# Performance work log

Hardware: AMD Instinct MI355X
Metric: run time of the kernel (lower is better)

Reference implementation:

```python
import jax, jax.numpy as jnp
import numpy as np

D = 768  # hidden dim hard-coded in the module


def setup_inputs() -> dict:
    key = jax.random.key(0)
    k1, k2, k3, k4, k5 = jax.random.split(key, 5)
    N, M = 512, 512
    return {
        "text_output": jax.random.normal(k1, (N, D), dtype=jnp.float32),
        "visual_output": jax.random.normal(k2, (M, D), dtype=jnp.float32),
        "W1": jax.random.normal(k3, (D, D), dtype=jnp.float32),
        "W2": jax.random.normal(k4, (D, D), dtype=jnp.float32),
        "W3": jax.random.normal(k5, (D, D), dtype=jnp.float32),
    }


def reference(text_output, visual_output, W1, W2, W3):
    # C[n,m] = tanh( (text @ W1) . visual[m] )
    C = jnp.tanh((text_output @ W1) @ visual_output.T)            # (N, M)
    W2_text = text_output @ W2                                    # (N, D)
    W3_visual = visual_output @ W3.T                              # (M, D)
    # M[n,m,:] = tanh(W2_text[n] + W3_visual[m] * C[n,m])
    Mt = jnp.tanh(W2_text[:, None, :] + W3_visual[None, :, :] * C[..., None])  # (N, M, D)
    # score[n,m] = text[n] . M[n,m]  (replaces the per-row Python loop)
    score = jnp.einsum("nd,nmd->nm", text_output, Mt)             # (N, M)
    return score
```

## Files before the change

### kernel.cpp

```cpp
#include <hip/hip_runtime.h>

#define DD   768
#define NN   512
#define MM   512

#define PRE_K 2.88539008177792681472f

typedef _Float16 h8 __attribute__((ext_vector_type(8)));
typedef __attribute__((ext_vector_type(4))) float f32x4;

__device__ __forceinline__ float fexp(float x) { return __builtin_amdgcn_exp2f(x); }
__device__ __forceinline__ float frcp(float x) { return __builtin_amdgcn_rcpf(x); }
__device__ __forceinline__ float fast_tanh(float x) {
  return 1.0f - 2.0f * frcp(fexp(PRE_K * x) + 1.0f);
}

__device__ __forceinline__ void splitf(float x, ushort& h, ushort& l) {
  const _Float16 hh = (_Float16)x;
  const _Float16 ll = (_Float16)(x - (float)hh);
  h = __builtin_bit_cast(unsigned short, hh);
  l = __builtin_bit_cast(unsigned short, ll);
}

__global__ __launch_bounds__(256) void prep_kernel(
    const float* __restrict__ text, const float* __restrict__ visual,
    const float* __restrict__ W1, const float* __restrict__ W2,
    const float* __restrict__ W3,
    ushort* __restrict__ th, ushort* __restrict__ tl,
    ushort* __restrict__ vh, ushort* __restrict__ vl,
    ushort* __restrict__ w3h, ushort* __restrict__ w3l,
    ushort* __restrict__ w1th, ushort* __restrict__ w1tl,
    ushort* __restrict__ w2th, ushort* __restrict__ w2tl,
    float* __restrict__ out)
{
  __shared__ float Lt[32][33];
  const int b = blockIdx.x;
  const int t = threadIdx.x;

  if (b < 1344) {
    const float* src; ushort *dh, *dl; size_t off;
    if (b < 384)      { src = text;   dh = th;  dl = tl;  off = (size_t)b * 1024; }
    else if (b < 768) { src = visual; dh = vh;  dl = vl;  off = (size_t)(b - 384) * 1024; }
    else              { src = W3;     dh = w3h; dl = w3l; off = (size_t)(b - 768) * 1024; }
    const size_t i = off + (size_t)t * 4;
    const float4 v = *(const float4*)&src[i];
    ushort4 h, l;
    splitf(v.x, h.x, l.x); splitf(v.y, h.y, l.y);
    splitf(v.z, h.z, l.z); splitf(v.w, h.w, l.w);
    *(ushort4*)&dh[i] = h;
    *(ushort4*)&dl[i] = l;
  } else if (b < 2496) {
    const int tt = b - 1344;
    const bool second = tt >= 576;
    const int tile = second ? tt - 576 : tt;
    const float* W = second ? W2 : W1;
    ushort* oh = second ? w2th : w1th;
    ushort* ol = second ? w2tl : w1tl;
    const int k0 = (tile / 24) * 32, j0 = (tile % 24) * 32;
    {
      const int k = t >> 3, j4 = (t & 7) * 4;
      const float4 v = *(const float4*)&W[(size_t)(k0 + k) * DD + j0 + j4];
      Lt[j4 + 0][k] = v.x; Lt[j4 + 1][k] = v.y;
      Lt[j4 + 2][k] = v.z; Lt[j4 + 3][k] = v.w;
    }
    __syncthreads();
    {
      const int j = t >> 3, k4 = (t & 7) * 4;
      ushort4 h, l;
      splitf(Lt[j][k4 + 0], h.x, l.x); splitf(Lt[j][k4 + 1], h.y, l.y);
      splitf(Lt[j][k4 + 2], h.z, l.z); splitf(Lt[j][k4 + 3], h.w, l.w);
      *(ushort4*)&oh[(size_t)(j0 + j) * DD + k0 + k4] = h;
      *(ushort4*)&ol[(size_t)(j0 + j) * DD + k0 + k4] = l;
    }
  } else {
    float* red = (float*)Lt;
    const int u = b - 2496;
    const int n0 = u * 2;
    const int half = t >> 7;
    const int lt = t & 127;

    const float* tr = text + (size_t)(n0 + half) * DD;
    float s = 0.f;
    #pragma unroll
    for (int i = 0; i < DD / 128; ++i) s += tr[lt + i * 128];
    red[t] = s;
    __syncthreads();
    #pragma unroll
    for (int st = 64; st > 0; st >>= 1) {
      if (lt < st) red[t] += red[t + st];
      __syncthreads();
    }
    const float Tn = red[half << 7];
    float4 o; o.x = Tn; o.y = Tn; o.z = Tn; o.w = Tn;
    *(float4*)&out[(size_t)(n0 + half) * MM + lt * 4] = o;
  }
}

#define BK   32
#define LROW 40
#define APL  (32 * LROW)
#define BPL  (64 * LROW)

template <bool ALO>
__device__ __forceinline__ void gemm_core32(
    ushort* __restrict__ As, ushort* __restrict__ Bs,
    const ushort* __restrict__ Ahg, const ushort* __restrict__ Alg,
    const ushort* __restrict__ Bhg, const ushort* __restrict__ Blg,
    int i0, int j0, int nsteps, f32x4* acc)
{
  const int tid = threadIdx.x;
  const int row = tid >> 2;
  const int ks8 = (tid & 3) * 8;
  const bool doA = (row < 32);
  const size_t ga = (size_t)(i0 + row) * DD + ks8;
  const size_t gb = (size_t)(j0 + row) * DD + ks8;
  const int lw = row * LROW + ks8;

  const int lane = tid & 63, wave = tid >> 6;
  const int r15 = lane & 15, quad = lane >> 4;
  const int wr = wave >> 1, wc = wave & 1;
  const int fa = (wr * 16 + r15) * LROW + quad * 8;
  const int fb = (wc * 32 + r15) * LROW + quad * 8;

  h8 pah, pal, pbh, pbl;
  if (doA) {
    pah = *(const h8*)(Ahg + ga);
    if (ALO) pal = *(const h8*)(Alg + ga);
  }
  pbh = *(const h8*)(Bhg + gb);
  pbl = *(const h8*)(Blg + gb);

  int p = 0;
  if (doA) {
    *(h8*)&As[lw] = pah;
    if (ALO) *(h8*)&As[APL + lw] = pal;
  }
  *(h8*)&Bs[lw] = pbh;
  *(h8*)&Bs[BPL + lw] = pbl;
  __syncthreads();

  for (int s = 0; s < nsteps; ++s) {
    const bool more = (s + 1 < nsteps);
    if (more) {
      if (doA) {
        pah = *(const h8*)(Ahg + ga + (s + 1) * BK);
        if (ALO) pal = *(const h8*)(Alg + ga + (s + 1) * BK);
      }
      pbh = *(const h8*)(Bhg + gb + (s + 1) * BK);
      pbl = *(const h8*)(Blg + gb + (s + 1) * BK);
    }
    ushort* Ac = As + p * 2 * APL;
    ushort* Bc = Bs + p * 2 * BPL;
    const h8 a_h = *(const h8*)&Ac[fa];
    h8 a_l; if (ALO) a_l = *(const h8*)&Ac[APL + fa];
    h8 b_h[2], b_l[2];
    #pragma unroll
    for (int c = 0; c < 2; ++c) {
      b_h[c] = *(const h8*)&Bc[fb + c * 16 * LROW];
      b_l[c] = *(const h8*)&Bc[BPL + fb + c * 16 * LROW];
    }
    #pragma unroll
    for (int c = 0; c < 2; ++c)
      acc[c] = __builtin_amdgcn_mfma_f32_16x16x32_f16(a_h, b_h[c], acc[c], 0, 0, 0);
    #pragma unroll
    for (int c = 0; c < 2; ++c)
      acc[c] = __builtin_amdgcn_mfma_f32_16x16x32_f16(a_h, b_l[c], acc[c], 0, 0, 0);
    if (ALO) {
      #pragma unroll
      for (int c = 0; c < 2; ++c)
        acc[c] = __builtin_amdgcn_mfma_f32_16x16x32_f16(a_l, b_h[c], acc[c], 0, 0, 0);
    }
    if (more) {
      const int q = p ^ 1;
      ushort* An = As + q * 2 * APL;
      ushort* Bn = Bs + q * 2 * BPL;
      if (doA) {
        *(h8*)&An[lw] = pah;
        if (ALO) *(h8*)&An[APL + lw] = pal;
      }
      *(h8*)&Bn[lw] = pbh;
      *(h8*)&Bn[BPL + lw] = pbl;
    }
    __syncthreads();
    p ^= 1;
  }
}

__global__ __launch_bounds__(256) void mfma1_kernel(
    const ushort* __restrict__ th, const ushort* __restrict__ tl,
    const ushort* __restrict__ vh, const ushort* __restrict__ vl,
    const ushort* __restrict__ w1th, const ushort* __restrict__ w1tl,
    const ushort* __restrict__ w2th, const ushort* __restrict__ w2tl,
    const ushort* __restrict__ w3h, const ushort* __restrict__ w3l,
    ushort* __restrict__ Ah, ushort* __restrict__ Al,
    float* __restrict__ kw2t, float* __restrict__ kw3v)
{
  __shared__ ushort As[2 * 2 * APL];
  __shared__ ushort Bs[2 * 2 * BPL];

  const int z  = blockIdx.z;
  const int j0 = blockIdx.x * 64;
  const int i0 = blockIdx.y * 32;

  f32x4 acc[2];
  acc[0] = (f32x4){0.f, 0.f, 0.f, 0.f};
  acc[1] = (f32x4){0.f, 0.f, 0.f, 0.f};

  if (z == 0)
    gemm_core32<true >(As, Bs, th, tl, w1th, w1tl, i0, j0, DD / BK, acc);
  else if (z == 1)
    gemm_core32<false>(As, Bs, th, tl, w2th, w2tl, i0, j0, DD / BK, acc);
  else
    gemm_core32<false>(As, Bs, vh, vl, w3h,  w3l,  i0, j0, DD / BK, acc);

  const int lane = threadIdx.x & 63, wave = threadIdx.x >> 6;
  const int r15 = lane & 15, quad = lane >> 4;
  const int wr = wave >> 1, wc = wave & 1;
  if (z == 0) {
    #pragma unroll
    for (int c = 0; c < 2; ++c)
      #pragma unroll
      for (int r = 0; r < 4; ++r) {
        const size_t o = (size_t)(i0 + wr * 16 + quad * 4 + r) * DD
                       + j0 + wc * 32 + c * 16 + r15;
        splitf(acc[c][r], Ah[o], Al[o]);
      }
  } else {
    float* Out = (z == 1) ? kw2t : kw3v;
    #pragma unroll
    for (int c = 0; c < 2; ++c)
      #pragma unroll
      for (int r = 0; r < 4; ++r)
        Out[(size_t)(i0 + wr * 16 + quad * 4 + r) * DD + j0 + wc * 32 + c * 16 + r15] =
            acc[c][r] * PRE_K;
  }
}

#define DCH    64
#define DRANGE 256
#define MLDW   68

__global__ __launch_bounds__(256) void main_kernel(
    const float* __restrict__ text, const float* __restrict__ kw2t,
    const float* __restrict__ kw3v,
    const ushort* __restrict__ Ah, const ushort* __restrict__ Al,
    const ushort* __restrict__ vh, const ushort* __restrict__ vl,
    float* __restrict__ out)
{
  __shared__ float sbuf[2][32 * MLDW];

  const int tid = threadIdx.x;
  const int nl = tid >> 4;
  const int ml = tid & 15;
  const int n0 = blockIdx.y * 16;
  const int m0 = blockIdx.x * 32;
  const int z  = blockIdx.z;
  const int lane = tid & 63, wave = tid >> 6;
  const int r15 = lane & 15, quad = lane >> 4;

  const size_t aoff  = (size_t)(n0 + r15) * DD + wave * (DD / 4) + quad * 8;
  const size_t b0off = (size_t)(m0 + r15) * DD + wave * (DD / 4) + quad * 8;
  const size_t b1off = (size_t)(m0 + 16 + r15) * DD + wave * (DD / 4) + quad * 8;
  const ushort* Ap  = Ah + aoff;
  const ushort* Alp = Al + aoff;
  const ushort* B0h = vh + b0off;
  const ushort* B0l = vl + b0off;
  const ushort* B1h = vh + b1off;
  const ushort* B1l = vl + b1off;

  f32x4 q0 = {0.f, 0.f, 0.f, 0.f}, q1 = {0.f, 0.f, 0.f, 0.f};
  h8 cah  = *(const h8*)Ap;
  h8 cal  = *(const h8*)Alp;
  h8 cb0h = *(const h8*)B0h;
  h8 cb0l = *(const h8*)B0l;
  h8 cb1h = *(const h8*)B1h;
  h8 cb1l = *(const h8*)B1l;
  #pragma unroll
  for (int s = 0; s < (DD / 4) / BK; ++s) {
    h8 nah, nal, nb0h, nb0l, nb1h, nb1l;
    const bool more = (s + 1 < (DD / 4) / BK);
    if (more) {
      nah  = *(const h8*)(Ap  + (s + 1) * BK);
      nal  = *(const h8*)(Alp + (s + 1) * BK);
      nb0h = *(const h8*)(B0h + (s + 1) * BK);
      nb0l = *(const h8*)(B0l + (s + 1) * BK);
      nb1h = *(const h8*)(B1h + (s + 1) * BK);
      nb1l = *(const h8*)(B1l + (s + 1) * BK);
    }
    q0 = __builtin_amdgcn_mfma_f32_16x16x32_f16(cah, cb0h, q0, 0, 0, 0);
    q1 = __builtin_amdgcn_mfma_f32_16x16x32_f16(cah, cb1h, q1, 0, 0, 0);
    q0 = __builtin_amdgcn_mfma_f32_16x16x32_f16(cah, cb0l, q0, 0, 0, 0);
    q1 = __builtin_amdgcn_mfma_f32_16x16x32_f16(cah, cb1l, q1, 0, 0, 0);
    q0 = __builtin_amdgcn_mfma_f32_16x16x32_f16(cal, cb0h, q0, 0, 0, 0);
    q1 = __builtin_amdgcn_mfma_f32_16x16x32_f16(cal, cb1h, q1, 0, 0, 0);
    if (more) { cah = nah; cal = nal; cb0h = nb0h; cb0l = nb0l; cb1h = nb1h; cb1l = nb1l; }
  }

  float (*Qs)[16][33] = (float (*)[16][33])(&sbuf[0][0]);
  #pragma unroll
  for (int r = 0; r < 4; ++r) {
    Qs[wave][quad * 4 + r][r15]      = q0[r];
    Qs[wave][quad * 4 + r][16 + r15] = q1[r];
  }
  __syncthreads();
  float sA = Qs[0][nl][ml];
  sA += Qs[1][nl][ml]; sA += Qs[2][nl][ml]; sA += Qs[3][nl][ml];
  float sB = Qs[0][nl][ml + 16];
  sB += Qs[1][nl][ml + 16]; sB += Qs[2][nl][ml + 16]; sB += Qs[3][nl][ml + 16];
  const float cA = fast_tanh(sA);
  const float cB = fast_tanh(sB);
  __syncthreads();

  const int n  = n0 + nl;
  const int mA = m0 + ml, mB = mA + 16;
  const int dbase = z * DRANGE;

  float4 aA = {0.f, 0.f, 0.f, 0.f};
  float4 aB = {0.f, 0.f, 0.f, 0.f};

  const float* gt = &text[(size_t)n * DD + dbase];
  const float* g2 = &kw2t[(size_t)n * DD + dbase];

  const int srow = tid >> 4;
  const int sc4  = (tid & 15) << 2;
  const float* g3a = &kw3v[(size_t)(m0 + srow) * DD + dbase + sc4];
  const float* g3b = &kw3v[(size_t)(m0 + 16 + srow) * DD + dbase + sc4];
  const int w3a = srow * MLDW + sc4;
  const int w3b = (16 + srow) * MLDW + sc4;

  float4 r3a = *(const float4*)g3a;
  float4 r3b = *(const float4*)g3b;
  int p = 0;
  *(float4*)&sbuf[0][w3a] = r3a;
  *(float4*)&sbuf[0][w3b] = r3b;
  __syncthreads();

  #pragma unroll
  for (int c = 0; c < DRANGE / DCH; ++c) {
    const bool more = (c + 1 < DRANGE / DCH);
    if (more) {
      r3a = *(const float4*)(g3a + (c + 1) * DCH);
      r3b = *(const float4*)(g3b + (c + 1) * DCH);
    }
    const float* bp = sbuf[p];
    const float* gtc = gt + c * DCH;
    const float* g2c = g2 + c * DCH;
    #pragma unroll 4
    for (int j = 0; j < DCH; j += 4) {
      const float4 tv  = *(const float4*)&gtc[j];
      const float4 w2v = *(const float4*)&g2c[j];
      const float4 w3A = *(const float4*)&bp[ml * MLDW + j];
      const float4 w3B = *(const float4*)&bp[(16 + ml) * MLDW + j];
      aA.x = fmaf(tv.x, frcp(fexp(fmaf(w3A.x, cA, w2v.x)) + 1.0f), aA.x);
      aA.y = fmaf(tv.y, frcp(fexp(fmaf(w3A.y, cA, w2v.y)) + 1.0f), aA.y);
      aA.z = fmaf(tv.z, frcp(fexp(fmaf(w3A.z, cA, w2v.z)) + 1.0f), aA.z);
      aA.w = fmaf(tv.w, frcp(fexp(fmaf(w3A.w, cA, w2v.w)) + 1.0f), aA.w);
      aB.x = fmaf(tv.x, frcp(fexp(fmaf(w3B.x, cB, w2v.x)) + 1.0f), aB.x);
      aB.y = fmaf(tv.y, frcp(fexp(fmaf(w3B.y, cB, w2v.y)) + 1.0f), aB.y);
      aB.z = fmaf(tv.z, frcp(fexp(fmaf(w3B.z, cB, w2v.z)) + 1.0f), aB.z);
      aB.w = fmaf(tv.w, frcp(fexp(fmaf(w3B.w, cB, w2v.w)) + 1.0f), aB.w);
    }
    if (more) {
      const int q = p ^ 1;
      *(float4*)&sbuf[q][w3a] = r3a;
      *(float4*)&sbuf[q][w3b] = r3b;
    }
    __syncthreads();
    p ^= 1;
  }

  float* op = out + (size_t)n * MM;
  unsafeAtomicAdd(&op[mA], -2.0f * ((aA.x + aA.y) + (aA.z + aA.w)));
  unsafeAtomicAdd(&op[mB], -2.0f * ((aB.x + aB.y) + (aB.z + aB.w)));
}

extern "C" void kernel_launch(void* const* d_in, const int* in_sizes, int n_in,
                              void* d_out, int out_size, void* d_ws, size_t ws_size,
                              hipStream_t stream) {
  const float* text   = (const float*)d_in[0];
  const float* visual = (const float*)d_in[1];
  const float* W1     = (const float*)d_in[2];
  const float* W2     = (const float*)d_in[3];
  const float* W3     = (const float*)d_in[4];
  float* out = (float*)d_out;

  char* base = (char*)d_ws;
  ushort* th   = (ushort*)(base);
  ushort* tl   = (ushort*)(base + 786432);
  ushort* vh   = (ushort*)(base + 1572864);
  ushort* vl   = (ushort*)(base + 2359296);
  ushort* w1th = (ushort*)(base + 3145728);
  ushort* w1tl = (ushort*)(base + 4325376);
  ushort* w2th = (ushort*)(base + 5505024);
  ushort* w2tl = (ushort*)(base + 6684672);
  ushort* w3h  = (ushort*)(base + 7864320);
  ushort* w3l  = (ushort*)(base + 9043968);
  ushort* Ah   = (ushort*)(base + 10223616);
  ushort* Al   = (ushort*)(base + 11010048);
  float*  kw2t = (float*) (base + 11796480);
  float*  kw3v = (float*) (base + 13369344);

  hipLaunchKernelGGL(prep_kernel, dim3(2752), dim3(256), 0, stream,
                     text, visual, W1, W2, W3,
                     th, tl, vh, vl, w3h, w3l, w1th, w1tl, w2th, w2tl, out);
  hipLaunchKernelGGL(mfma1_kernel, dim3(DD / 64, NN / 32, 3), dim3(256), 0, stream,
                     th, tl, vh, vl, w1th, w1tl, w2th, w2tl, w3h, w3l,
                     Ah, Al, kw2t, kw3v);
  hipLaunchKernelGGL(main_kernel, dim3(MM / 32, NN / 16, 3), dim3(256), 0, stream,
                     text, kw2t, kw3v, Ah, Al, vh, vl, out);
}
```

Before: 142.3 us.

## Merge three kernels into one cooperative persistent kernel with grid syncs

New measurement: 480.0 us. 237% more time.

```diff
diff --git a/kernel.cpp b/kernel.cpp
--- a/kernel.cpp
+++ b/kernel.cpp
@@ -1,4 +1,7 @@
 #include <hip/hip_runtime.h>
+#include <hip/hip_cooperative_groups.h>
+
+namespace cg = cooperative_groups;
 
 #define DD   768
 #define NN   512
@@ -22,80 +25,6 @@
   l = __builtin_bit_cast(unsigned short, ll);
 }
 
-__global__ __launch_bounds__(256) void prep_kernel(
-    const float* __restrict__ text, const float* __restrict__ visual,
-    const float* __restrict__ W1, const float* __restrict__ W2,
-    const float* __restrict__ W3,
-    ushort* __restrict__ th, ushort* __restrict__ tl,
-    ushort* __restrict__ vh, ushort* __restrict__ vl,
-    ushort* __restrict__ w3h, ushort* __restrict__ w3l,
-    ushort* __restrict__ w1th, ushort* __restrict__ w1tl,
-    ushort* __restrict__ w2th, ushort* __restrict__ w2tl,
-    float* __restrict__ out)
-{
-  __shared__ float Lt[32][33];
-  const int b = blockIdx.x;
-  const int t = threadIdx.x;
-
-  if (b < 1344) {
-    const float* src; ushort *dh, *dl; size_t off;
-    if (b < 384)      { src = text;   dh = th;  dl = tl;  off = (size_t)b * 1024; }
-    else if (b < 768) { src = visual; dh = vh;  dl = vl;  off = (size_t)(b - 384) * 1024; }
-    else              { src = W3;     dh = w3h; dl = w3l; off = (size_t)(b - 768) * 1024; }
-    const size_t i = off + (size_t)t * 4;
-    const float4 v = *(const float4*)&src[i];
-    ushort4 h, l;
-    splitf(v.x, h.x, l.x); splitf(v.y, h.y, l.y);
-    splitf(v.z, h.z, l.z); splitf(v.w, h.w, l.w);
-    *(ushort4*)&dh[i] = h;
-    *(ushort4*)&dl[i] = l;
-  } else if (b < 2496) {
-    const int tt = b - 1344;
-    const bool second = tt >= 576;
-    const int tile = second ? tt - 576 : tt;
-    const float* W = second ? W2 : W1;
-    ushort* oh = second ? w2th : w1th;
-    ushort* ol = second ? w2tl : w1tl;
-    const int k0 = (tile / 24) * 32, j0 = (tile % 24) * 32;
-    {
-      const int k = t >> 3, j4 = (t & 7) * 4;
-      const float4 v = *(const float4*)&W[(size_t)(k0 + k) * DD + j0 + j4];
-      Lt[j4 + 0][k] = v.x; Lt[j4 + 1][k] = v.y;
-      Lt[j4 + 2][k] = v.z; Lt[j4 + 3][k] = v.w;
-    }
-    __syncthreads();
-    {
-      const int j = t >> 3, k4 = (t & 7) * 4;
-      ushort4 h, l;
-      splitf(Lt[j][k4 + 0], h.x, l.x); splitf(Lt[j][k4 + 1], h.y, l.y);
-      splitf(Lt[j][k4 + 2], h.z, l.z); splitf(Lt[j][k4 + 3], h.w, l.w);
-      *(ushort4*)&oh[(size_t)(j0 + j) * DD + k0 + k4] = h;
-      *(ushort4*)&ol[(size_t)(j0 + j) * DD + k0 + k4] = l;
-    }
-  } else {
-    float* red = (float*)Lt;
-    const int u = b - 2496;
-    const int n0 = u * 2;
-    const int half = t >> 7;
-    const int lt = t & 127;
-
-    const float* tr = text + (size_t)(n0 + half) * DD;
-    float s = 0.f;
-    #pragma unroll
-    for (int i = 0; i < DD / 128; ++i) s += tr[lt + i * 128];
-    red[t] = s;
-    __syncthreads();
-    #pragma unroll
-    for (int st = 64; st > 0; st >>= 1) {
-      if (lt < st) red[t] += red[t + st];
-      __syncthreads();
-    }
-    const float Tn = red[half << 7];
-    float4 o; o.x = Tn; o.y = Tn; o.z = Tn; o.w = Tn;
-    *(float4*)&out[(size_t)(n0 + half) * MM + lt * 4] = o;
-  }
-}
-
 #define BK   32
 #define LROW 40
 #define APL  (32 * LROW)
@@ -103,17 +32,17 @@
 
 template <bool ALO>
 __device__ __forceinline__ void gemm_core32(
-    ushort* __restrict__ As, ushort* __restrict__ Bs,
-    const ushort* __restrict__ Ahg, const ushort* __restrict__ Alg,
-    const ushort* __restrict__ Bhg, const ushort* __restrict__ Blg,
-    int i0, int j0, int nsteps, f32x4* acc)
+    ushort* As, ushort* Bs,
+    const ushort* Ahg, const ushort* Alg,
+    const ushort* Bhg, const ushort* Blg,
+    int i0, int j0, int k0, int nsteps, f32x4* acc)
 {
   const int tid = threadIdx.x;
   const int row = tid >> 2;
   const int ks8 = (tid & 3) * 8;
   const bool doA = (row < 32);
-  const size_t ga = (size_t)(i0 + row) * DD + ks8;
-  const size_t gb = (size_t)(j0 + row) * DD + ks8;
+  const size_t ga = (size_t)(i0 + row) * DD + k0 + ks8;
+  const size_t gb = (size_t)(j0 + row) * DD + k0 + ks8;
   const int lw = row * LROW + ks8;
 
   const int lane = tid & 63, wave = tid >> 6;
@@ -186,192 +115,249 @@
   }
 }
 
-__global__ __launch_bounds__(256) void mfma1_kernel(
-    const ushort* __restrict__ th, const ushort* __restrict__ tl,
-    const ushort* __restrict__ vh, const ushort* __restrict__ vl,
-    const ushort* __restrict__ w1th, const ushort* __restrict__ w1tl,
-    const ushort* __restrict__ w2th, const ushort* __restrict__ w2tl,
-    const ushort* __restrict__ w3h, const ushort* __restrict__ w3l,
+#define DCH    64
+#define DRANGE 192
+#define MLDW   68
+#define SMEM_BYTES 34816
+
+__global__ __launch_bounds__(256, 4) void mega_kernel(
+    const float* __restrict__ text, const float* __restrict__ visual,
+    const float* __restrict__ W1, const float* __restrict__ W2,
+    const float* __restrict__ W3,
+    ushort* __restrict__ th, ushort* __restrict__ tl,
+    ushort* __restrict__ vh, ushort* __restrict__ vl,
+    ushort* __restrict__ w3h, ushort* __restrict__ w3l,
+    ushort* w1th, ushort* w1tl,
+    ushort* w2th, ushort* w2tl,
     ushort* __restrict__ Ah, ushort* __restrict__ Al,
-    float* __restrict__ kw2t, float* __restrict__ kw3v)
-{
-  __shared__ ushort As[2 * 2 * APL];
-  __shared__ ushort Bs[2 * 2 * BPL];
-
-  const int z  = blockIdx.z;
-  const int j0 = blockIdx.x * 64;
-  const int i0 = blockIdx.y * 32;
-
-  f32x4 acc[2];
-  acc[0] = (f32x4){0.f, 0.f, 0.f, 0.f};
-  acc[1] = (f32x4){0.f, 0.f, 0.f, 0.f};
-
-  if (z == 0)
-    gemm_core32<true >(As, Bs, th, tl, w1th, w1tl, i0, j0, DD / BK, acc);
-  else if (z == 1)
-    gemm_core32<false>(As, Bs, th, tl, w2th, w2tl, i0, j0, DD / BK, acc);
-  else
-    gemm_core32<false>(As, Bs, vh, vl, w3h,  w3l,  i0, j0, DD / BK, acc);
-
-  const int lane = threadIdx.x & 63, wave = threadIdx.x >> 6;
-  const int r15 = lane & 15, quad = lane >> 4;
-  const int wr = wave >> 1, wc = wave & 1;
-  if (z == 0) {
-    #pragma unroll
-    for (int c = 0; c < 2; ++c)
-      #pragma unroll
-      for (int r = 0; r < 4; ++r) {
-        const size_t o = (size_t)(i0 + wr * 16 + quad * 4 + r) * DD
-                       + j0 + wc * 32 + c * 16 + r15;
-        splitf(acc[c][r], Ah[o], Al[o]);
-      }
-  } else {
-    float* Out = (z == 1) ? kw2t : kw3v;
-    #pragma unroll
-    for (int c = 0; c < 2; ++c)
-      #pragma unroll
-      for (int r = 0; r < 4; ++r)
-        Out[(size_t)(i0 + wr * 16 + quad * 4 + r) * DD + j0 + wc * 32 + c * 16 + r15] =
-            acc[c][r] * PRE_K;
-  }
-}
-
-#define DCH    64
-#define DRANGE 256
-#define MLDW   68
-
-__global__ __launch_bounds__(256) void main_kernel(
-    const float* __restrict__ text, const float* __restrict__ kw2t,
-    const float* __restrict__ kw3v,
-    const ushort* __restrict__ Ah, const ushort* __restrict__ Al,
-    const ushort* __restrict__ vh, const ushort* __restrict__ vl,
+    float* __restrict__ kw2t, float* __restrict__ kw3v,
+    float* Q,
     float* __restrict__ out)
 {
-  __shared__ float sbuf[2][32 * MLDW];
-
-  const int tid = threadIdx.x;
-  const int nl = tid >> 4;
-  const int ml = tid & 15;
-  const int n0 = blockIdx.y * 16;
-  const int m0 = blockIdx.x * 32;
-  const int z  = blockIdx.z;
-  const int lane = tid & 63, wave = tid >> 6;
-  const int r15 = lane & 15, quad = lane >> 4;
-
-  const size_t aoff  = (size_t)(n0 + r15) * DD + wave * (DD / 4) + quad * 8;
-  const size_t b0off = (size_t)(m0 + r15) * DD + wave * (DD / 4) + quad * 8;
-  const size_t b1off = (size_t)(m0 + 16 + r15) * DD + wave * (DD / 4) + quad * 8;
-  const ushort* Ap  = Ah + aoff;
-  const ushort* Alp = Al + aoff;
-  const ushort* B0h = vh + b0off;
-  const ushort* B0l = vl + b0off;
-  const ushort* B1h = vh + b1off;
-  const ushort* B1l = vl + b1off;
-
-  f32x4 q0 = {0.f, 0.f, 0.f, 0.f}, q1 = {0.f, 0.f, 0.f, 0.f};
-  h8 cah  = *(const h8*)Ap;
-  h8 cal  = *(const h8*)Alp;
-  h8 cb0h = *(const h8*)B0h;
-  h8 cb0l = *(const h8*)B0l;
-  h8 cb1h = *(const h8*)B1h;
-  h8 cb1l = *(const h8*)B1l;
-  #pragma unroll
-  for (int s = 0; s < (DD / 4) / BK; ++s) {
-    h8 nah, nal, nb0h, nb0l, nb1h, nb1l;
-    const bool more = (s + 1 < (DD / 4) / BK);
-    if (more) {
-      nah  = *(const h8*)(Ap  + (s + 1) * BK);
-      nal  = *(const h8*)(Alp + (s + 1) * BK);
-      nb0h = *(const h8*)(B0h + (s + 1) * BK);
-      nb0l = *(const h8*)(B0l + (s + 1) * BK);
-      nb1h = *(const h8*)(B1h + (s + 1) * BK);
-      nb1l = *(const h8*)(B1l + (s + 1) * BK);
-    }
-    q0 = __builtin_amdgcn_mfma_f32_16x16x32_f16(cah, cb0h, q0, 0, 0, 0);
-    q1 = __builtin_amdgcn_mfma_f32_16x16x32_f16(cah, cb1h, q1, 0, 0, 0);
-    q0 = __builtin_amdgcn_mfma_f32_16x16x32_f16(cah, cb0l, q0, 0, 0, 0);
-    q1 = __builtin_amdgcn_mfma_f32_16x16x32_f16(cah, cb1l, q1, 0, 0, 0);
-    q0 = __builtin_amdgcn_mfma_f32_16x16x32_f16(cal, cb0h, q0, 0, 0, 0);
-    q1 = __builtin_amdgcn_mfma_f32_16x16x32_f16(cal, cb1h, q1, 0, 0, 0);
-    if (more) { cah = nah; cal = nal; cb0h = nb0h; cb0l = nb0l; cb1h = nb1h; cb1l = nb1l; }
-  }
-
-  float (*Qs)[16][33] = (float (*)[16][33])(&sbuf[0][0]);
-  #pragma unroll
-  for (int r = 0; r < 4; ++r) {
-    Qs[wave][quad * 4 + r][r15]      = q0[r];
-    Qs[wave][quad * 4 + r][16 + r15] = q1[r];
-  }
-  __syncthreads();
-  float sA = Qs[0][nl][ml];
-  sA += Qs[1][nl][ml]; sA += Qs[2][nl][ml]; sA += Qs[3][nl][ml];
-  float sB = Qs[0][nl][ml + 16];
-  sB += Qs[1][nl][ml + 16]; sB += Qs[2][nl][ml + 16]; sB += Qs[3][nl][ml + 16];
-  const float cA = fast_tanh(sA);
-  const float cB = fast_tanh(sB);
-  __syncthreads();
-
-  const int n  = n0 + nl;
-  const int mA = m0 + ml, mB = mA + 16;
-  const int dbase = z * DRANGE;
-
-  float4 aA = {0.f, 0.f, 0.f, 0.f};
-  float4 aB = {0.f, 0.f, 0.f, 0.f};
-
-  const float* gt = &text[(size_t)n * DD + dbase];
-  const float* g2 = &kw2t[(size_t)n * DD + dbase];
-
-  const int srow = tid >> 4;
-  const int sc4  = (tid & 15) << 2;
-  const float* g3a = &kw3v[(size_t)(m0 + srow) * DD + dbase + sc4];
-  const float* g3b = &kw3v[(size_t)(m0 + 16 + srow) * DD + dbase + sc4];
-  const int w3a = srow * MLDW + sc4;
-  const int w3b = (16 + srow) * MLDW + sc4;
-
-  float4 r3a = *(const float4*)g3a;
-  float4 r3b = *(const float4*)g3b;
-  int p = 0;
-  *(float4*)&sbuf[0][w3a] = r3a;
-  *(float4*)&sbuf[0][w3b] = r3b;
-  __syncthreads();
-
-  #pragma unroll
-  for (int c = 0; c < DRANGE / DCH; ++c) {
-    const bool more = (c + 1 < DRANGE / DCH);
-    if (more) {
-      r3a = *(const float4*)(g3a + (c + 1) * DCH);
-      r3b = *(const float4*)(g3b + (c + 1) * DCH);
-    }
-    const float* bp = sbuf[p];
-    const float* gtc = gt + c * DCH;
-    const float* g2c = g2 + c * DCH;
-    #pragma unroll 4
-    for (int j = 0; j < DCH; j += 4) {
-      const float4 tv  = *(const float4*)&gtc[j];
-      const float4 w2v = *(const float4*)&g2c[j];
-      const float4 w3A = *(const float4*)&bp[ml * MLDW + j];
-      const float4 w3B = *(const float4*)&bp[(16 + ml) * MLDW + j];
-      aA.x = fmaf(tv.x, frcp(fexp(fmaf(w3A.x, cA, w2v.x)) + 1.0f), aA.x);
-      aA.y = fmaf(tv.y, frcp(fexp(fmaf(w3A.y, cA, w2v.y)) + 1.0f), aA.y);
-      aA.z = fmaf(tv.z, frcp(fexp(fmaf(w3A.z, cA, w2v.z)) + 1.0f), aA.z);
-      aA.w = fmaf(tv.w, frcp(fexp(fmaf(w3A.w, cA, w2v.w)) + 1.0f), aA.w);
-      aB.x = fmaf(tv.x, frcp(fexp(fmaf(w3B.x, cB, w2v.x)) + 1.0f), aB.x);
-      aB.y = fmaf(tv.y, frcp(fexp(fmaf(w3B.y, cB, w2v.y)) + 1.0f), aB.y);
-      aB.z = fmaf(tv.z, frcp(fexp(fmaf(w3B.z, cB, w2v.z)) + 1.0f), aB.z);
-      aB.w = fmaf(tv.w, frcp(fexp(fmaf(w3B.w, cB, w2v.w)) + 1.0f), aB.w);
-    }
-    if (more) {
-      const int q = p ^ 1;
-      *(float4*)&sbuf[q][w3a] = r3a;
-      *(float4*)&sbuf[q][w3b] = r3b;
-    }
-    __syncthreads();
-    p ^= 1;
-  }
-
-  float* op = out + (size_t)n * MM;
-  unsafeAtomicAdd(&op[mA], -2.0f * ((aA.x + aA.y) + (aA.z + aA.w)));
-  unsafeAtomicAdd(&op[mB], -2.0f * ((aB.x + aB.y) + (aB.z + aB.w)));
+  __shared__ __align__(16) char smem[SMEM_BYTES];
+  cg::grid_group grid = cg::this_grid();
+  const int t  = threadIdx.x;
+  const int nb = gridDim.x;
+
+  {
+    float (*Lt)[33] = (float (*)[33])smem;
+    for (int b = blockIdx.x; b < 2752; b += nb) {
+      if (b < 1344) {
+        const float* src; ushort *dh, *dl; size_t off;
+        if (b < 384)      { src = text;   dh = th;  dl = tl;  off = (size_t)b * 1024; }
+        else if (b < 768) { src = visual; dh = vh;  dl = vl;  off = (size_t)(b - 384) * 1024; }
+        else              { src = W3;     dh = w3h; dl = w3l; off = (size_t)(b - 768) * 1024; }
+        const size_t i = off + (size_t)t * 4;
+        const float4 v = *(const float4*)&src[i];
+        ushort4 h, l;
+        splitf(v.x, h.x, l.x); splitf(v.y, h.y, l.y);
+        splitf(v.z, h.z, l.z); splitf(v.w, h.w, l.w);
+        *(ushort4*)&dh[i] = h;
+        *(ushort4*)&dl[i] = l;
+      } else if (b < 2496) {
+        const int tt = b - 1344;
+        const bool second = tt >= 576;
+        const int tile = second ? tt - 576 : tt;
+        const float* W = second ? W2 : W1;
+        ushort* oh = second ? w2th : w1th;
+        ushort* ol = second ? w2tl : w1tl;
+        const int k0 = (tile / 24) * 32, j0 = (tile % 24) * 32;
+        {
+          const int k = t >> 3, j4 = (t & 7) * 4;
+          const float4 v = *(const float4*)&W[(size_t)(k0 + k) * DD + j0 + j4];
+          Lt[j4 + 0][k] = v.x; Lt[j4 + 1][k] = v.y;
+          Lt[j4 + 2][k] = v.z; Lt[j4 + 3][k] = v.w;
+        }
+        __syncthreads();
+        {
+          const int j = t >> 3, k4 = (t & 7) * 4;
+          ushort4 h, l;
+          splitf(Lt[j][k4 + 0], h.x, l.x); splitf(Lt[j][k4 + 1], h.y, l.y);
+          splitf(Lt[j][k4 + 2], h.z, l.z); splitf(Lt[j][k4 + 3], h.w, l.w);
+          *(ushort4*)&oh[(size_t)(j0 + j) * DD + k0 + k4] = h;
+          *(ushort4*)&ol[(size_t)(j0 + j) * DD + k0 + k4] = l;
+        }
+      } else {
+        float* red = (float*)smem;
+        const int u = b - 2496;
+        const int n0 = u * 2;
+        const int half = t >> 7;
+        const int lt = t & 127;
+        const float* tr = text + (size_t)(n0 + half) * DD;
+        float s = 0.f;
+        #pragma unroll
+        for (int i = 0; i < DD / 128; ++i) s += tr[lt + i * 128];
+        red[t] = s;
+        __syncthreads();
+        #pragma unroll
+        for (int st = 64; st > 0; st >>= 1) {
+          if (lt < st) red[t] += red[t + st];
+          __syncthreads();
+        }
+        const float Tn = red[half << 7];
+        float4 o; o.x = Tn; o.y = Tn; o.z = Tn; o.w = Tn;
+        *(float4*)&out[(size_t)(n0 + half) * MM + lt * 4] = o;
+      }
+      __syncthreads();
+    }
+  }
+  __threadfence();
+  grid.sync();
+
+  {
+    ushort* As = (ushort*)smem;
+    ushort* Bs = (ushort*)(smem + 10240);
+    const int lane = t & 63, wave = t >> 6;
+    const int r15 = lane & 15, quad = lane >> 4;
+    const int wr = wave >> 1, wc = wave & 1;
+    for (int u = blockIdx.x; u < 576; u += nb) {
+      const int z = u / 192, rem = u % 192;
+      const int j0 = (rem % 12) * 64, i0 = (rem / 12) * 32;
+      f32x4 acc[2];
+      acc[0] = (f32x4){0.f, 0.f, 0.f, 0.f};
+      acc[1] = (f32x4){0.f, 0.f, 0.f, 0.f};
+      if (z == 0)
+        gemm_core32<true >(As, Bs, th, tl, w1th, w1tl, i0, j0, 0, DD / BK, acc);
+      else if (z == 1)
+        gemm_core32<false>(As, Bs, th, tl, w2th, w2tl, i0, j0, 0, DD / BK, acc);
+      else
+        gemm_core32<false>(As, Bs, vh, vl, w3h,  w3l,  i0, j0, 0, DD / BK, acc);
+      if (z == 0) {
+        #pragma unroll
+        for (int c = 0; c < 2; ++c)
+          #pragma unroll
+          for (int r = 0; r < 4; ++r) {
+            const size_t o = (size_t)(i0 + wr * 16 + quad * 4 + r) * DD
+                           + j0 + wc * 32 + c * 16 + r15;
+            splitf(acc[c][r], Ah[o], Al[o]);
+          }
+      } else {
+        float* Out = (z == 1) ? kw2t : kw3v;
+        #pragma unroll
+        for (int c = 0; c < 2; ++c)
+          #pragma unroll
+          for (int r = 0; r < 4; ++r)
+            Out[(size_t)(i0 + wr * 16 + quad * 4 + r) * DD + j0 + wc * 32 + c * 16 + r15] =
+                acc[c][r] * PRE_K;
+      }
+    }
+  }
+  __threadfence();
+  grid.sync();
+
+  {
+    ushort* As = (ushort*)smem;
+    ushort* Bs = (ushort*)(smem + 10240);
+    const int lane = t & 63, wave = t >> 6;
+    const int r15 = lane & 15, quad = lane >> 4;
+    const int wr = wave >> 1, wc = wave & 1;
+    for (int u = blockIdx.x; u < 512; u += nb) {
+      const int z = u >> 7, rem = u & 127;
+      const int j0 = (rem & 7) * 64, i0 = (rem >> 3) * 32;
+      f32x4 acc[2];
+      acc[0] = (f32x4){0.f, 0.f, 0.f, 0.f};
+      acc[1] = (f32x4){0.f, 0.f, 0.f, 0.f};
+      gemm_core32<true>(As, Bs, Ah, Al, vh, vl, i0, j0, z * (DD / 4), (DD / 4) / BK, acc);
+      float* Qp = Q + (size_t)z * NN * MM;
+      #pragma unroll
+      for (int c = 0; c < 2; ++c)
+        #pragma unroll
+        for (int r = 0; r < 4; ++r)
+          Qp[(size_t)(i0 + wr * 16 + quad * 4 + r) * MM + j0 + wc * 32 + c * 16 + r15] =
+              acc[c][r];
+    }
+  }
+  __threadfence();
+  grid.sync();
+
+  {
+    float* sb = (float*)smem;
+    const int nl = t >> 4;
+    const int ml = t & 15;
+    for (int u = blockIdx.x; u < 2048; u += nb) {
+      const int z  = u >> 9;
+      const int rem = u & 511;
+      const int m0 = (rem & 15) * 32;
+      const int n0 = (rem >> 4) * 16;
+      const int n  = n0 + nl;
+      const int mA = m0 + ml, mB = mA + 16;
+      const int dbase = z * DRANGE;
+
+      float cA = 0.f, cB = 0.f;
+      #pragma unroll
+      for (int zz = 0; zz < 4; ++zz) {
+        const float* q = Q + (size_t)zz * NN * MM + (size_t)n * MM;
+        cA += q[mA]; cB += q[mB];
+      }
+      cA = fast_tanh(cA); cB = fast_tanh(cB);
+
+      float4 aA = {0.f, 0.f, 0.f, 0.f};
+      float4 aB = {0.f, 0.f, 0.f, 0.f};
+
+      const int srow = t >> 4;
+      const int sc4  = (t & 15) << 2;
+      const float* gt  = &text[(size_t)(n0 + srow) * DD + dbase + sc4];
+      const float* g2  = &kw2t[(size_t)(n0 + srow) * DD + dbase + sc4];
+      const float* g3a = &kw3v[(size_t)(m0 + srow) * DD + dbase + sc4];
+      const float* g3b = &kw3v[(size_t)(m0 + 16 + srow) * DD + dbase + sc4];
+      const int wt  = srow * MLDW + sc4;
+      const int w2  = (16 + srow) * MLDW + sc4;
+      const int w3a = (32 + srow) * MLDW + sc4;
+      const int w3b = (48 + srow) * MLDW + sc4;
+
+      float4 rt  = *(const float4*)gt;
+      float4 r2  = *(const float4*)g2;
+      float4 r3a = *(const float4*)g3a;
+      float4 r3b = *(const float4*)g3b;
+      int p = 0;
+      *(float4*)&sb[wt]  = rt;
+      *(float4*)&sb[w2]  = r2;
+      *(float4*)&sb[w3a] = r3a;
+      *(float4*)&sb[w3b] = r3b;
+      __syncthreads();
+
+      #pragma unroll
+      for (int c = 0; c < DRANGE / DCH; ++c) {
+        const bool more = (c + 1 < DRANGE / DCH);
+        if (more) {
+          rt  = *(const float4*)(gt  + (c + 1) * DCH);
+          r2  = *(const float4*)(g2  + (c + 1) * DCH);
+          r3a = *(const float4*)(g3a + (c + 1) * DCH);
+          r3b = *(const float4*)(g3b + (c + 1) * DCH);
+        }
+        const float* bp = sb + p * (64 * MLDW);
+        #pragma unroll 4
+        for (int j = 0; j < DCH; j += 4) {
+          const float4 tv  = *(const float4*)&bp[nl * MLDW + j];
+          const float4 w2v = *(const float4*)&bp[(16 + nl) * MLDW + j];
+          const float4 w3A = *(const float4*)&bp[(32 + ml) * MLDW + j];
+          const float4 w3B = *(const float4*)&bp[(48 + ml) * MLDW + j];
+          aA.x = fmaf(tv.x, frcp(fexp(fmaf(w3A.x, cA, w2v.x)) + 1.0f), aA.x);
+          aA.y = fmaf(tv.y, frcp(fexp(fmaf(w3A.y, cA, w2v.y)) + 1.0f), aA.y);
+          aA.z = fmaf(tv.z, frcp(fexp(fmaf(w3A.z, cA, w2v.z)) + 1.0f), aA.z);
+          aA.w = fmaf(tv.w, frcp(fexp(fmaf(w3A.w, cA, w2v.w)) + 1.0f), aA.w);
+          aB.x = fmaf(tv.x, frcp(fexp(fmaf(w3B.x, cB, w2v.x)) + 1.0f), aB.x);
+          aB.y = fmaf(tv.y, frcp(fexp(fmaf(w3B.y, cB, w2v.y)) + 1.0f), aB.y);
+          aB.z = fmaf(tv.z, frcp(fexp(fmaf(w3B.z, cB, w2v.z)) + 1.0f), aB.z);
+          aB.w = fmaf(tv.w, frcp(fexp(fmaf(w3B.w, cB, w2v.w)) + 1.0f), aB.w);
+        }
+        if (more) {
+          const int q = p ^ 1;
+          float* nbuf = sb + q * (64 * MLDW);
+          *(float4*)&nbuf[wt]  = rt;
+          *(float4*)&nbuf[w2]  = r2;
+          *(float4*)&nbuf[w3a] = r3a;
+          *(float4*)&nbuf[w3b] = r3b;
+        }
+        __syncthreads();
+        p ^= 1;
+      }
+
+      float* op = out + (size_t)n * MM;
+      unsafeAtomicAdd(&op[mA], -2.0f * ((aA.x + aA.y) + (aA.z + aA.w)));
+      unsafeAtomicAdd(&op[mB], -2.0f * ((aB.x + aB.y) + (aB.z + aB.w)));
+    }
+  }
 }
 
 extern "C" void kernel_launch(void* const* d_in, const int* in_sizes, int n_in,
@@ -399,13 +385,22 @@
   ushort* Al   = (ushort*)(base + 11010048);
   float*  kw2t = (float*) (base + 11796480);
   float*  kw3v = (float*) (base + 13369344);
-
-  hipLaunchKernelGGL(prep_kernel, dim3(2752), dim3(256), 0, stream,
-                     text, visual, W1, W2, W3,
-                     th, tl, vh, vl, w3h, w3l, w1th, w1tl, w2th, w2tl, out);
-  hipLaunchKernelGGL(mfma1_kernel, dim3(DD / 64, NN / 32, 3), dim3(256), 0, stream,
-                     th, tl, vh, vl, w1th, w1tl, w2th, w2tl, w3h, w3l,
-                     Ah, Al, kw2t, kw3v);
-  hipLaunchKernelGGL(main_kernel, dim3(MM / 32, NN / 16, 3), dim3(256), 0, stream,
-                     text, kw2t, kw3v, Ah, Al, vh, vl, out);
+  float*  Q    = (ws_size >= (size_t)19136512) ? (float*)(base + 14942208)
+                                               : (float*)(base + 3145728);
+
+  int maxb = 0;
+  hipOccupancyMaxActiveBlocksPerMultiprocessor(&maxb, mega_kernel, 256, 0);
+  if (maxb < 1) maxb = 1;
+  int grid = maxb * 256;
+  if (grid > 1024) grid = 1024;
+
+  void* args[] = {
+    (void*)&text, (void*)&visual, (void*)&W1, (void*)&W2, (void*)&W3,
+    (void*)&th, (void*)&tl, (void*)&vh, (void*)&vl,
+    (void*)&w3h, (void*)&w3l, (void*)&w1th, (void*)&w1tl,
+    (void*)&w2th, (void*)&w2tl, (void*)&Ah, (void*)&Al,
+    (void*)&kw2t, (void*)&kw3v, (void*)&Q, (void*)&out
+  };
+  hipLaunchCooperativeKernel((const void*)mega_kernel, dim3(grid), dim3(256),
+                             args, 0, stream);
 }
```

## Split C-score GEMM into separate split-K kernel and stage text/W2 in LDS

Applied to the files above, without the earlier changes.

Measured after the change: 145.0 us. Within noise of the previous version (+1.9%).

```diff
diff --git a/kernel.cpp b/kernel.cpp
--- a/kernel.cpp
+++ b/kernel.cpp
@@ -106,14 +106,14 @@
     ushort* __restrict__ As, ushort* __restrict__ Bs,
     const ushort* __restrict__ Ahg, const ushort* __restrict__ Alg,
     const ushort* __restrict__ Bhg, const ushort* __restrict__ Blg,
-    int i0, int j0, int nsteps, f32x4* acc)
+    int i0, int j0, int k0, int nsteps, f32x4* acc)
 {
   const int tid = threadIdx.x;
   const int row = tid >> 2;
   const int ks8 = (tid & 3) * 8;
   const bool doA = (row < 32);
-  const size_t ga = (size_t)(i0 + row) * DD + ks8;
-  const size_t gb = (size_t)(j0 + row) * DD + ks8;
+  const size_t ga = (size_t)(i0 + row) * DD + k0 + ks8;
+  const size_t gb = (size_t)(j0 + row) * DD + k0 + ks8;
   const int lw = row * LROW + ks8;
 
   const int lane = tid & 63, wave = tid >> 6;
@@ -207,11 +207,11 @@
   acc[1] = (f32x4){0.f, 0.f, 0.f, 0.f};
 
   if (z == 0)
-    gemm_core32<true >(As, Bs, th, tl, w1th, w1tl, i0, j0, DD / BK, acc);
+    gemm_core32<true >(As, Bs, th, tl, w1th, w1tl, i0, j0, 0, DD / BK, acc);
   else if (z == 1)
-    gemm_core32<false>(As, Bs, th, tl, w2th, w2tl, i0, j0, DD / BK, acc);
+    gemm_core32<false>(As, Bs, th, tl, w2th, w2tl, i0, j0, 0, DD / BK, acc);
   else
-    gemm_core32<false>(As, Bs, vh, vl, w3h,  w3l,  i0, j0, DD / BK, acc);
+    gemm_core32<false>(As, Bs, vh, vl, w3h,  w3l,  i0, j0, 0, DD / BK, acc);
 
   const int lane = threadIdx.x & 63, wave = threadIdx.x >> 6;
   const int r15 = lane & 15, quad = lane >> 4;
@@ -236,18 +236,45 @@
   }
 }
 
-#define DCH    64
-#define DRANGE 256
-#define MLDW   68
-
-__global__ __launch_bounds__(256) void main_kernel(
-    const float* __restrict__ text, const float* __restrict__ kw2t,
-    const float* __restrict__ kw3v,
+__global__ __launch_bounds__(256) void mfma2_kernel(
     const ushort* __restrict__ Ah, const ushort* __restrict__ Al,
     const ushort* __restrict__ vh, const ushort* __restrict__ vl,
+    float* __restrict__ Q)
+{
+  __shared__ ushort As[2 * 2 * APL];
+  __shared__ ushort Bs[2 * 2 * BPL];
+
+  const int z  = blockIdx.z;
+  const int j0 = blockIdx.x * 64;
+  const int i0 = blockIdx.y * 32;
+
+  f32x4 acc[2];
+  acc[0] = (f32x4){0.f, 0.f, 0.f, 0.f};
+  acc[1] = (f32x4){0.f, 0.f, 0.f, 0.f};
+  gemm_core32<true>(As, Bs, Ah, Al, vh, vl, i0, j0, z * (DD / 4), (DD / 4) / BK, acc);
+
+  const int lane = threadIdx.x & 63, wave = threadIdx.x >> 6;
+  const int r15 = lane & 15, quad = lane >> 4;
+  const int wr = wave >> 1, wc = wave & 1;
+  float* Qp = Q + (size_t)z * NN * MM;
+  #pragma unroll
+  for (int c = 0; c < 2; ++c)
+    #pragma unroll
+    for (int r = 0; r < 4; ++r)
+      Qp[(size_t)(i0 + wr * 16 + quad * 4 + r) * MM + j0 + wc * 32 + c * 16 + r15] =
+          acc[c][r];
+}
+
+#define DCH    32
+#define DRANGE 192
+#define MLDW   36
+
+__global__ __launch_bounds__(256, 8) void main_kernel(
+    const float* __restrict__ text, const float* __restrict__ kw2t,
+    const float* __restrict__ kw3v, const float* __restrict__ Q,
     float* __restrict__ out)
 {
-  __shared__ float sbuf[2][32 * MLDW];
+  __shared__ float sbuf[2][64 * MLDW];
 
   const int tid = threadIdx.x;
   const int nl = tid >> 4;
@@ -255,102 +282,51 @@
   const int n0 = blockIdx.y * 16;
   const int m0 = blockIdx.x * 32;
   const int z  = blockIdx.z;
-  const int lane = tid & 63, wave = tid >> 6;
-  const int r15 = lane & 15, quad = lane >> 4;
-
-  const size_t aoff  = (size_t)(n0 + r15) * DD + wave * (DD / 4) + quad * 8;
-  const size_t b0off = (size_t)(m0 + r15) * DD + wave * (DD / 4) + quad * 8;
-  const size_t b1off = (size_t)(m0 + 16 + r15) * DD + wave * (DD / 4) + quad * 8;
-  const ushort* Ap  = Ah + aoff;
-  const ushort* Alp = Al + aoff;
-  const ushort* B0h = vh + b0off;
-  const ushort* B0l = vl + b0off;
-  const ushort* B1h = vh + b1off;
-  const ushort* B1l = vl + b1off;
-
-  f32x4 q0 = {0.f, 0.f, 0.f, 0.f}, q1 = {0.f, 0.f, 0.f, 0.f};
-  h8 cah  = *(const h8*)Ap;
-  h8 cal  = *(const h8*)Alp;
-  h8 cb0h = *(const h8*)B0h;
-  h8 cb0l = *(const h8*)B0l;
-  h8 cb1h = *(const h8*)B1h;
-  h8 cb1l = *(const h8*)B1l;
-  #pragma unroll
-  for (int s = 0; s < (DD / 4) / BK; ++s) {
-    h8 nah, nal, nb0h, nb0l, nb1h, nb1l;
-    const bool more = (s + 1 < (DD / 4) / BK);
-    if (more) {
-      nah  = *(const h8*)(Ap  + (s + 1) * BK);
-      nal  = *(const h8*)(Alp + (s + 1) * BK);
-      nb0h = *(const h8*)(B0h + (s + 1) * BK);
-      nb0l = *(const h8*)(B0l + (s + 1) * BK);
-      nb1h = *(const h8*)(B1h + (s + 1) * BK);
-      nb1l = *(const h8*)(B1l + (s + 1) * BK);
-    }
-    q0 = __builtin_amdgcn_mfma_f32_16x16x32_f16(cah, cb0h, q0, 0, 0, 0);
-    q1 = __builtin_amdgcn_mfma_f32_16x16x32_f16(cah, cb1h, q1, 0, 0, 0);
-    q0 = __builtin_amdgcn_mfma_f32_16x16x32_f16(cah, cb0l, q0, 0, 0, 0);
-    q1 = __builtin_amdgcn_mfma_f32_16x16x32_f16(cah, cb1l, q1, 0, 0, 0);
-    q0 = __builtin_amdgcn_mfma_f32_16x16x32_f16(cal, cb0h, q0, 0, 0, 0);
-    q1 = __builtin_amdgcn_mfma_f32_16x16x32_f16(cal, cb1h, q1, 0, 0, 0);
-    if (more) { cah = nah; cal = nal; cb0h = nb0h; cb0l = nb0l; cb1h = nb1h; cb1l = nb1l; }
-  }
-
-  float (*Qs)[16][33] = (float (*)[16][33])(&sbuf[0][0]);
-  #pragma unroll
-  for (int r = 0; r < 4; ++r) {
-    Qs[wave][quad * 4 + r][r15]      = q0[r];
-    Qs[wave][quad * 4 + r][16 + r15] = q1[r];
-  }
-  __syncthreads();
-  float sA = Qs[0][nl][ml];
-  sA += Qs[1][nl][ml]; sA += Qs[2][nl][ml]; sA += Qs[3][nl][ml];
-  float sB = Qs[0][nl][ml + 16];
-  sB += Qs[1][nl][ml + 16]; sB += Qs[2][nl][ml + 16]; sB += Qs[3][nl][ml + 16];
-  const float cA = fast_tanh(sA);
-  const float cB = fast_tanh(sB);
-  __syncthreads();
-
   const int n  = n0 + nl;
   const int mA = m0 + ml, mB = mA + 16;
   const int dbase = z * DRANGE;
 
+  float cA = 0.f, cB = 0.f;
+  #pragma unroll
+  for (int zz = 0; zz < 4; ++zz) {
+    const float* q = Q + (size_t)zz * NN * MM + (size_t)n * MM;
+    cA += q[mA]; cB += q[mB];
+  }
+  cA = fast_tanh(cA); cB = fast_tanh(cB);
+
   float4 aA = {0.f, 0.f, 0.f, 0.f};
   float4 aB = {0.f, 0.f, 0.f, 0.f};
 
-  const float* gt = &text[(size_t)n * DD + dbase];
-  const float* g2 = &kw2t[(size_t)n * DD + dbase];
-
-  const int srow = tid >> 4;
-  const int sc4  = (tid & 15) << 2;
-  const float* g3a = &kw3v[(size_t)(m0 + srow) * DD + dbase + sc4];
-  const float* g3b = &kw3v[(size_t)(m0 + 16 + srow) * DD + dbase + sc4];
-  const int w3a = srow * MLDW + sc4;
-  const int w3b = (16 + srow) * MLDW + sc4;
-
-  float4 r3a = *(const float4*)g3a;
-  float4 r3b = *(const float4*)g3b;
+  const int srow = tid >> 3;
+  const int sc   = (tid & 7) << 2;
+  const float* g1 = (srow < 16)
+      ? &text[(size_t)(n0 + srow) * DD + dbase + sc]
+      : &kw2t[(size_t)(n0 + srow - 16) * DD + dbase + sc];
+  const float* g3 = &kw3v[(size_t)(m0 + srow) * DD + dbase + sc];
+  const int w1 = srow * MLDW + sc;
+  const int w3 = (32 + srow) * MLDW + sc;
+
+  float4 r1 = *(const float4*)g1;
+  float4 r3 = *(const float4*)g3;
   int p = 0;
-  *(float4*)&sbuf[0][w3a] = r3a;
-  *(float4*)&sbuf[0][w3b] = r3b;
+  *(float4*)&sbuf[0][w1] = r1;
+  *(float4*)&sbuf[0][w3] = r3;
   __syncthreads();
 
   #pragma unroll
   for (int c = 0; c < DRANGE / DCH; ++c) {
     const bool more = (c + 1 < DRANGE / DCH);
     if (more) {
-      r3a = *(const float4*)(g3a + (c + 1) * DCH);
-      r3b = *(const float4*)(g3b + (c + 1) * DCH);
+      r1 = *(const float4*)(g1 + (c + 1) * DCH);
+      r3 = *(const float4*)(g3 + (c + 1) * DCH);
     }
     const float* bp = sbuf[p];
-    const float* gtc = gt + c * DCH;
-    const float* g2c = g2 + c * DCH;
     #pragma unroll 4
     for (int j = 0; j < DCH; j += 4) {
-      const float4 tv  = *(const float4*)&gtc[j];
-      const float4 w2v = *(const float4*)&g2c[j];
-      const float4 w3A = *(const float4*)&bp[ml * MLDW + j];
-      const float4 w3B = *(const float4*)&bp[(16 + ml) * MLDW + j];
+      const float4 tv  = *(const float4*)&bp[nl * MLDW + j];
+      const float4 w2v = *(const float4*)&bp[(16 + nl) * MLDW + j];
+      const float4 w3A = *(const float4*)&bp[(32 + ml) * MLDW + j];
+      const float4 w3B = *(const float4*)&bp[(48 + ml) * MLDW + j];
       aA.x = fmaf(tv.x, frcp(fexp(fmaf(w3A.x, cA, w2v.x)) + 1.0f), aA.x);
       aA.y = fmaf(tv.y, frcp(fexp(fmaf(w3A.y, cA, w2v.y)) + 1.0f), aA.y);
       aA.z = fmaf(tv.z, frcp(fexp(fmaf(w3A.z, cA, w2v.z)) + 1.0f), aA.z);
@@ -362,8 +338,8 @@
     }
     if (more) {
       const int q = p ^ 1;
-      *(float4*)&sbuf[q][w3a] = r3a;
-      *(float4*)&sbuf[q][w3b] = r3b;
+      *(float4*)&sbuf[q][w1] = r1;
+      *(float4*)&sbuf[q][w3] = r3;
     }
     __syncthreads();
     p ^= 1;
@@ -399,6 +375,7 @@
   ushort* Al   = (ushort*)(base + 11010048);
   float*  kw2t = (float*) (base + 11796480);
   float*  kw3v = (float*) (base + 13369344);
+  float*  Q    = (float*) (base + 3145728);
 
   hipLaunchKernelGGL(prep_kernel, dim3(2752), dim3(256), 0, stream,
                      text, visual, W1, W2, W3,
@@ -406,6 +383,8 @@
   hipLaunchKernelGGL(mfma1_kernel, dim3(DD / 64, NN / 32, 3), dim3(256), 0, stream,
                      th, tl, vh, vl, w1th, w1tl, w2th, w2tl, w3h, w3l,
                      Ah, Al, kw2t, kw3v);
-  hipLaunchKernelGGL(main_kernel, dim3(MM / 32, NN / 16, 3), dim3(256), 0, stream,
-                     text, kw2t, kw3v, Ah, Al, vh, vl, out);
-}
+  hipLaunchKernelGGL(mfma2_kernel, dim3(MM / 64, NN / 32, 4), dim3(256), 0, stream,
+                     Ah, Al, vh, vl, Q);
+  hipLaunchKernelGGL(main_kernel, dim3(MM / 32, NN / 16, 4), dim3(256), 0, stream,
+                     text, kw2t, kw3v, Q, out);
+}
```
